# Optimization experiments

Measured on AMD Instinct MI355X. Metric: run time of the kernel, lower is better.

## Reference

```python
import jax, jax.numpy as jnp
import numpy as np

H, KV, HD = 16, 8, 128           # heads, kv heads, head_dim
THETA, EPS = 1.0e6, 1e-6         # rope theta, rmsnorm eps
QMAX = 127.0                     # symmetric int8


def qdq(x):
    """Symmetric int8 fake quant-dequant along last dim (per-token / per-out-channel)."""
    s = jnp.maximum(jnp.max(jnp.abs(x), axis=-1, keepdims=True) / QMAX, 1e-8)
    q = jnp.clip(jnp.round(x / s), -QMAX, QMAX) * s
    return x + jax.lax.stop_gradient(q - x)  # STE


def rms_norm(x, w):
    v = jnp.mean(jnp.square(x.astype(jnp.float32)), axis=-1, keepdims=True)
    return (x.astype(jnp.float32) * jax.lax.rsqrt(v + EPS)).astype(x.dtype) * w


def rotate_half(x):
    x1, x2 = jnp.split(x, 2, axis=-1)
    return jnp.concatenate([-x2, x1], axis=-1)


def setup_inputs() -> dict:
    key = jax.random.key(0)
    ks = jax.random.split(key, 6)
    B, S, D = 1, 2048, 2048
    return {
        "hidden_states": jax.random.normal(ks[0], (B, S, D), jnp.float32),
        "Wq": jax.random.normal(ks[1], (H * HD, D), jnp.float32) * 0.02,
        "Wk": jax.random.normal(ks[2], (KV * HD, D), jnp.float32) * 0.02,
        "Wv": jax.random.normal(ks[3], (KV * HD, D), jnp.float32) * 0.02,
        "Wo": jax.random.normal(ks[4], (D, H * HD), jnp.float32) * 0.02,
        "q_norm_w": jnp.ones((HD,), jnp.float32),
        "k_norm_w": jnp.ones((HD,), jnp.float32),
        "position_ids": jnp.arange(S, dtype=jnp.int32)[None, :],
    }


def reference(hidden_states, Wq, Wk, Wv, Wo, q_norm_w, k_norm_w, position_ids):
    B, S, D = hidden_states.shape
    xq = qdq(hidden_states)                                  # per-token act quant (shared input)
    q = (xq @ qdq(Wq).T).reshape(B, S, H, HD).transpose(0, 2, 1, 3)   # [B,H,S,hd]
    k = (xq @ qdq(Wk).T).reshape(B, S, KV, HD).transpose(0, 2, 1, 3)  # [B,KV,S,hd]
    v = (xq @ qdq(Wv).T).reshape(B, S, KV, HD).transpose(0, 2, 1, 3)

    q = rms_norm(q, q_norm_w)
    k = rms_norm(k, k_norm_w)

    # rotary embeddings
    inv = 1.0 / (THETA ** (jnp.arange(0, HD, 2, dtype=jnp.float32) / HD))
    freqs = position_ids.astype(jnp.float32)[..., None] * inv          # [B,S,hd/2]
    emb = jnp.concatenate([freqs, freqs], axis=-1)                     # [B,S,hd]
    cos = jnp.cos(emb)[:, None].astype(q.dtype)                        # [B,1,S,hd]
    sin = jnp.sin(emb)[:, None].astype(q.dtype)
    q = q * cos + rotate_half(q) * sin
    k = k * cos + rotate_half(k) * sin

    # qkt_matmul.quant_x1 / quant_x2
    q = qdq(q)
    k = qdq(k)

    # GQA repeat
    g = H // KV
    k = jnp.repeat(k, g, axis=1)
    v = jnp.repeat(v, g, axis=1)

    scores = jnp.einsum("bhqd,bhkd->bhqk", q, k) * (HD ** -0.5)       # [B,H,S,S]
    causal = jnp.tril(jnp.ones((S, S), bool))
    scores = jnp.where(causal[None, None], scores, jnp.float32(-1e9))
    p = jax.nn.softmax(scores.astype(jnp.float32), axis=-1).astype(q.dtype)

    # pv_matmul.quant_x1 / quant_x2
    p = qdq(p)
    v = qdq(v)
    attn = jnp.einsum("bhqk,bhkd->bhqd", p, v)                        # [B,H,S,hd]
    attn = attn.transpose(0, 2, 1, 3).reshape(B, S, H * HD)
    return qdq(attn) @ qdq(Wo).T
```

## Files before the change

### kernel.cpp

```cpp
#include <hip/hip_runtime.h>
#include <math.h>

#define NH 16
#define NKV 8
#define HDIM 128
#define SEQ 2048
#define DMODEL 2048

typedef int   v4i __attribute__((ext_vector_type(4)));
typedef float v4f __attribute__((ext_vector_type(4)));
typedef _Float16 v8h __attribute__((ext_vector_type(8)));

static constexpr float SM_SCALE = 0.08838834764831843f;

#define GLOBP(p) (__attribute__((address_space(1))) void*)(p)
#define LDSP(p)  (__attribute__((address_space(3))) void*)(p)
#define ASYNC16(g, l) __builtin_amdgcn_global_load_lds(GLOBP(g), LDSP(l), 16, 0, 0)


__device__ __forceinline__ unsigned short f2h_bits(float x) {
    _Float16 h = (_Float16)x;
    return __builtin_bit_cast(unsigned short, h);
}

__global__ __launch_bounds__(256) void quant_all_k(const float* __restrict__ hidden,
        const float* __restrict__ Wq, const float* __restrict__ Wk,
        const float* __restrict__ Wv, const float* __restrict__ Wo,
        signed char* __restrict__ out, float* __restrict__ scale) {
    int p = blockIdx.x;
    int row0g = p * 16;
    const float* in; int lr0;
    if (row0g < 2048)      { in = hidden; lr0 = row0g; }
    else if (row0g < 4096) { in = Wq; lr0 = row0g - 2048; }
    else if (row0g < 5120) { in = Wk; lr0 = row0g - 4096; }
    else if (row0g < 6144) { in = Wv; lr0 = row0g - 5120; }
    else                   { in = Wo; lr0 = row0g - 6144; }
    const int cols = 2048;
    int tid = threadIdx.x;
    __shared__ float srow[16];
    int r = tid >> 4, l16 = tid & 15;
    const float4* x4 = (const float4*)(in + (size_t)(lr0 + r) * cols);
    float amax = 0.f;
    for (int c4 = l16; c4 < (cols >> 2); c4 += 16) {
        float4 v = x4[c4];
        amax = fmaxf(amax, fmaxf(fmaxf(fabsf(v.x), fabsf(v.y)),
                                 fmaxf(fabsf(v.z), fabsf(v.w))));
    }
#pragma unroll
    for (int m = 1; m <= 8; m <<= 1) amax = fmaxf(amax, __shfl_xor(amax, m));
    if (l16 == 0) {
        float s = fmaxf(amax / 127.0f, 1e-8f);
        srow[r] = s;
        scale[row0g + r] = s;
    }
    __syncthreads();
    int total = (cols >> 4) * 16;
    size_t obase = (size_t)p * 32768;
    for (int idx = tid; idx < total; idx += 256) {
        int f = idx >> 6, q = (idx >> 4) & 3, rr = idx & 15;
        const float* src = in + (size_t)(lr0 + rr) * cols + f * 64 + q * 16;
        float s = srow[rr];
        unsigned int wds[4];
#pragma unroll
        for (int g = 0; g < 4; ++g) {
            float4 v = *(const float4*)(src + g * 4);
            int b0 = (int)fminf(fmaxf(rintf(v.x / s), -127.f), 127.f);
            int b1 = (int)fminf(fmaxf(rintf(v.y / s), -127.f), 127.f);
            int b2 = (int)fminf(fmaxf(rintf(v.z / s), -127.f), 127.f);
            int b3 = (int)fminf(fmaxf(rintf(v.w / s), -127.f), 127.f);
            wds[g] = (b0 & 255) | ((b1 & 255) << 8) | ((b2 & 255) << 16) | ((b3 & 255) << 24);
        }
        *(uint4*)(out + obase + (size_t)idx * 16) =
            make_uint4(wds[0], wds[1], wds[2], wds[3]);
    }
}

__global__ __launch_bounds__(256) void row_quant_k(const float* __restrict__ in,
        signed char* __restrict__ out, float* __restrict__ scale, int cols) {
    int row0 = blockIdx.x * 16;
    int tid = threadIdx.x;
    __shared__ float srow[16];
    int r = tid >> 4, l16 = tid & 15;
    const float4* x4 = (const float4*)(in + (size_t)(row0 + r) * cols);
    float amax = 0.f;
    for (int c4 = l16; c4 < (cols >> 2); c4 += 16) {
        float4 v = x4[c4];
        amax = fmaxf(amax, fmaxf(fmaxf(fabsf(v.x), fabsf(v.y)),
                                 fmaxf(fabsf(v.z), fabsf(v.w))));
    }
#pragma unroll
    for (int m = 1; m <= 8; m <<= 1) amax = fmaxf(amax, __shfl_xor(amax, m));
    if (l16 == 0) {
        float s = fmaxf(amax / 127.0f, 1e-8f);
        srow[r] = s;
        scale[row0 + r] = s;
    }
    __syncthreads();
    int total = (cols >> 4) * 16;
    size_t obase = ((size_t)(row0 >> 4) * (cols >> 6)) << 10;
    for (int idx = tid; idx < total; idx += 256) {
        int f = idx >> 6, q = (idx >> 4) & 3, rr = idx & 15;
        const float* src = in + (size_t)(row0 + rr) * cols + f * 64 + q * 16;
        float s = srow[rr];
        unsigned int wds[4];
#pragma unroll
        for (int g = 0; g < 4; ++g) {
            float4 v = *(const float4*)(src + g * 4);
            int b0 = (int)fminf(fmaxf(rintf(v.x / s), -127.f), 127.f);
            int b1 = (int)fminf(fmaxf(rintf(v.y / s), -127.f), 127.f);
            int b2 = (int)fminf(fmaxf(rintf(v.z / s), -127.f), 127.f);
            int b3 = (int)fminf(fmaxf(rintf(v.w / s), -127.f), 127.f);
            wds[g] = (b0 & 255) | ((b1 & 255) << 8) | ((b2 & 255) << 16) | ((b3 & 255) << 24);
        }
        *(uint4*)(out + obase + (size_t)idx * 16) =
            make_uint4(wds[0], wds[1], wds[2], wds[3]);
    }
}

__global__ __launch_bounds__(256, 3) void gemm_i8_k(const signed char* __restrict__ A,
        const float* __restrict__ sa, const signed char* __restrict__ B,
        const float* __restrict__ sb, float* __restrict__ C, int M, int N, int K) {
    __shared__ __align__(16) signed char lsA[3][8192];
    __shared__ __align__(16) signed char lsB[3][8192];
    int tid = threadIdx.x;
    int w = tid >> 6, l = tid & 63;
    int wr = w >> 1, wc = w & 1;
    int lrow = l & 15;
    int m0 = blockIdx.y * 128, n0 = blockIdx.x * 128;
    int kb6 = K >> 6;
    v4i acc[4][4];
#pragma unroll
    for (int i = 0; i < 4; ++i)
#pragma unroll
        for (int j = 0; j < 4; ++j) acc[i][j] = (v4i){0, 0, 0, 0};

    auto stage = [&](int buf, int k6) {
#pragma unroll
        for (int a = 0; a < 2; ++a) {
            int f = a * 4 + w;
            ASYNC16(A + (((size_t)(((m0 >> 4) + f) * kb6 + k6)) << 10) + l * 16,
                    lsA[buf] + f * 1024);
            ASYNC16(B + (((size_t)(((n0 >> 4) + f) * kb6 + k6)) << 10) + l * 16,
                    lsB[buf] + f * 1024);
        }
    };

    stage(0, 0);
    if (kb6 > 1) {
        stage(1, 1);
        asm volatile("s_waitcnt vmcnt(4)" ::: "memory");
    } else {
        asm volatile("s_waitcnt vmcnt(0)" ::: "memory");
    }
    __builtin_amdgcn_s_barrier();
    for (int t = 0; t < kb6; ++t) {
        if (t + 2 < kb6) stage((t + 2) % 3, t + 2);
        int cur = t % 3;
        v4i af[4], bf[4];
#pragma unroll
        for (int i = 0; i < 4; ++i) af[i] = *(const v4i*)(lsA[cur] + (wr * 4 + i) * 1024 + l * 16);
#pragma unroll
        for (int j = 0; j < 4; ++j) bf[j] = *(const v4i*)(lsB[cur] + (wc * 4 + j) * 1024 + l * 16);
#pragma unroll
        for (int i = 0; i < 4; ++i)
#pragma unroll
            for (int j = 0; j < 4; ++j)
                acc[i][j] = __builtin_amdgcn_mfma_i32_16x16x64_i8(af[i], bf[j], acc[i][j], 0, 0, 0);
        if (t + 2 < kb6) asm volatile("s_waitcnt vmcnt(4)" ::: "memory");
        else             asm volatile("s_waitcnt vmcnt(0)" ::: "memory");
        __builtin_amdgcn_s_barrier();
    }
    int r0 = m0 + wr * 64, c0 = n0 + wc * 64;
    int lg = l >> 4;
    float sbv[4];
#pragma unroll
    for (int j = 0; j < 4; ++j) sbv[j] = sb[c0 + j * 16 + lrow];
#pragma unroll
    for (int i = 0; i < 4; ++i) {
        float4 s4 = *(const float4*)(sa + r0 + i * 16 + lg * 4);
        float sav[4] = {s4.x, s4.y, s4.z, s4.w};
#pragma unroll
        for (int j = 0; j < 4; ++j) {
#pragma unroll
            for (int reg = 0; reg < 4; ++reg) {
                int rr = r0 + i * 16 + lg * 4 + reg;
                C[(size_t)rr * N + c0 + j * 16 + lrow] = (float)acc[i][j][reg] * (sav[reg] * sbv[j]);
            }
        }
    }
}

__global__ void rope_init_k(float* __restrict__ inv_tab) {
    int i = threadIdx.x;
    inv_tab[i] = 1.0f / (float)pow(1.0e6, (double)i / 64.0);
}
__global__ void rope_tab_k(const int* __restrict__ pos_ids, const float* __restrict__ inv_tab,
                           float* __restrict__ ct, float* __restrict__ st) {
    int t = blockIdx.x;
    int fi = threadIdx.x;
    float fr = (float)pos_ids[t] * inv_tab[fi];
    float sn, c;
    sincosf(fr, &sn, &c);
    ct[t * 64 + fi] = c;
    st[t * 64 + fi] = sn;
}

__global__ __launch_bounds__(256) void qkv_post_k(const float* __restrict__ qkv_lin,
        const float* __restrict__ qw, const float* __restrict__ kw,
        const float* __restrict__ ct, const float* __restrict__ st,
        signed char* __restrict__ q_i8, float* __restrict__ sq,
        signed char* __restrict__ k_i8, float* __restrict__ sk) {
    int t = blockIdx.x;
    int wv = threadIdx.x >> 6, l = threadIdx.x & 63;
    const float* row = qkv_lin + (size_t)t * 4096;
    float cth = ct[t * 64 + l];
    float sth = st[t * 64 + l];
    size_t ta0 = (size_t)(((t >> 4) * 2) << 10)
               + (size_t)((((l >> 4) & 3) << 8) + ((t & 15) << 4) + (l & 15));
    for (int slot = wv; slot < 24; slot += 4) {
        float x0 = row[slot * 128 + l];
        float x1 = row[slot * 128 + l + 64];
        float ss = x0 * x0 + x1 * x1;
#pragma unroll
        for (int m = 1; m <= 32; m <<= 1) ss += __shfl_xor(ss, m);
        float rs = 1.0f / sqrtf(ss / 128.0f + 1e-6f);
        const float* wn = (slot < 16) ? qw : kw;
        x0 = (x0 * rs) * wn[l];
        x1 = (x1 * rs) * wn[l + 64];
        float nx0 = x0 * cth - x1 * sth;
        float nx1 = x1 * cth + x0 * sth;
        x0 = nx0; x1 = nx1;
        float amax = fmaxf(fabsf(x0), fabsf(x1));
#pragma unroll
        for (int m = 1; m <= 32; m <<= 1) amax = fmaxf(amax, __shfl_xor(amax, m));
        float s = fmaxf(amax / 127.0f, 1e-8f);
        float q0 = fminf(fmaxf(rintf(x0 / s), -127.f), 127.f);
        float q1 = fminf(fmaxf(rintf(x1 / s), -127.f), 127.f);
        if (slot < 16) {
            signed char* dst = q_i8 + (size_t)slot * (SEQ * 128);
            dst[ta0] = (signed char)(int)q0;
            dst[ta0 + 1024] = (signed char)(int)q1;
            if (l == 0) sq[slot * SEQ + t] = s;
        } else {
            signed char* dst = k_i8 + (size_t)(slot - 16) * (SEQ * 128);
            dst[ta0] = (signed char)(int)q0;
            dst[ta0 + 1024] = (signed char)(int)q1;
            if (l == 0) sk[(slot - 16) * SEQ + t] = s;
        }
    }
}

__global__ __launch_bounds__(256) void vt_split_k(const float* __restrict__ qkv_lin,
        unsigned short* __restrict__ vtT) {
    int kv = blockIdx.y, kb = blockIdx.x;
    int t0 = kb * 64;
    __shared__ float tile[64][132];
    __shared__ float srow[64];
    int tid = threadIdx.x;
    const float* src = qkv_lin + (size_t)t0 * 4096 + 3072 + kv * 128;
#pragma unroll
    for (int i = 0; i < 8; ++i) {
        int f4 = i * 256 + tid;
        int r = f4 >> 5, c = (f4 & 31) << 2;
        float4 v = *(const float4*)(src + (size_t)r * 4096 + c);
        tile[r][c] = v.x; tile[r][c + 1] = v.y; tile[r][c + 2] = v.z; tile[r][c + 3] = v.w;
    }
    __syncthreads();
    {
        int r = tid >> 2, qq = tid & 3;
        float amax = 0.f;
#pragma unroll
        for (int e = 0; e < 32; ++e) amax = fmaxf(amax, fabsf(tile[r][qq * 32 + e]));
        amax = fmaxf(amax, __shfl_xor(amax, 1));
        amax = fmaxf(amax, __shfl_xor(amax, 2));
        if (qq == 0) srow[r] = fmaxf(amax / 127.0f, 1e-8f);
    }
    __syncthreads();
    int d = tid >> 1, th = (tid & 1) * 32;
    size_t base = (size_t)kv * (SEQ * 128);
#pragma unroll
    for (int j = 0; j < 32; j += 2) {
        int tl = th + j;
        float s0 = srow[tl], s1 = srow[tl + 1];
        float a = fminf(fmaxf(rintf(tile[tl][d] / s0), -127.f), 127.f) * s0;
        float b = fminf(fmaxf(rintf(tile[tl + 1][d] / s1), -127.f), 127.f) * s1;
        unsigned int ua = f2h_bits(a), ub = f2h_bits(b);
        int off = kb * 8192 + ((d >> 4) * 2 + ((tl >> 5) & 1)) * 512
                + (((d & 15) + (((tl >> 3) & 3) << 4)) << 3) + (tl & 7);
        *(unsigned int*)(vtT + base + off) = ua | (ub << 16);
    }
}

__global__ __launch_bounds__(256, 4) void attn_p1_k(const signed char* __restrict__ q_i8,
        const float* __restrict__ sq, const signed char* __restrict__ k_i8,
        const float* __restrict__ sk, float* __restrict__ mm) {
    int bx = blockIdx.x, hp = blockIdx.y;
    int qb = 31 - (bx >> 2), c = bx & 3;
    int nch = (qb + 8) >> 3;
    if (c >= nch) return;
    int q0 = qb * 64;
    int kb0 = c * 8, kb1 = min((c + 1) * 8, qb + 1);
    int tid = threadIdx.x, w = tid >> 6, l = tid & 63;
    int lrow = l & 15, lg = l >> 4;
    int h0 = hp * 2, h1 = h0 + 1;

    const signed char* qtA = q_i8 + (size_t)h0 * (SEQ * 128)
                           + ((size_t)((((q0 >> 4) + w) * 2)) << 10) + l * 16;
    const signed char* qtB = qtA + (size_t)(SEQ * 128);
    v4i qfA0 = *(const v4i*)(qtA), qfA1 = *(const v4i*)(qtA + 1024);
    v4i qfB0 = *(const v4i*)(qtB), qfB1 = *(const v4i*)(qtB + 1024);
    float4 sA = *(const float4*)(sq + (size_t)h0 * SEQ + q0 + w * 16 + lg * 4);
    float4 sB = *(const float4*)(sq + (size_t)h1 * SEQ + q0 + w * 16 + lg * 4);
    float sqrA[4] = {sA.x, sA.y, sA.z, sA.w};
    float sqrB[4] = {sB.x, sB.y, sB.z, sB.w};
    const signed char* kbase = k_i8 + (size_t)hp * (SEQ * 128);
    const float* skb = sk + (size_t)hp * SEQ;

    float mA[4], mB[4];
#pragma unroll
    for (int r = 0; r < 4; ++r) { mA[r] = -1e30f; mB[r] = -1e30f; }

    v4i ka[8], kn[8];
    float skc[4], skn[4];
    auto loadK = [&](v4i* dst, float* sdst, int k0) {
#pragma unroll
        for (int f = 0; f < 8; ++f)
            dst[f] = *(const v4i*)(kbase + ((size_t)((k0 >> 4) * 2 + f) << 10) + l * 16);
#pragma unroll
        for (int j = 0; j < 4; ++j) sdst[j] = skb[k0 + j * 16 + lrow];
    };

    loadK(ka, skc, kb0 * 64);
    for (int kb = kb0; kb < kb1; ++kb) {
        if (kb + 1 < kb1) loadK(kn, skn, (kb + 1) * 64);
        int k0 = kb * 64;
        v4i sciA[4], sciB[4];
#pragma unroll
        for (int j = 0; j < 4; ++j) {
            v4i z = {0, 0, 0, 0};
            v4i tA = __builtin_amdgcn_mfma_i32_16x16x64_i8(qfA0, ka[j * 2], z, 0, 0, 0);
            sciA[j] = __builtin_amdgcn_mfma_i32_16x16x64_i8(qfA1, ka[j * 2 + 1], tA, 0, 0, 0);
            v4i tB = __builtin_amdgcn_mfma_i32_16x16x64_i8(qfB0, ka[j * 2], z, 0, 0, 0);
            sciB[j] = __builtin_amdgcn_mfma_i32_16x16x64_i8(qfB1, ka[j * 2 + 1], tB, 0, 0, 0);
        }
#pragma unroll
        for (int reg = 0; reg < 4; ++reg) {
            int r = q0 + w * 16 + lg * 4 + reg;
#pragma unroll
            for (int j = 0; j < 4; ++j) {
                bool ok = (k0 + j * 16 + lrow <= r);
                float ss = skc[j] * SM_SCALE;
                float svA = ((float)sciA[j][reg] * sqrA[reg]) * ss;
                float svB = ((float)sciB[j][reg] * sqrB[reg]) * ss;
                mA[reg] = fmaxf(mA[reg], ok ? svA : -1e30f);
                mB[reg] = fmaxf(mB[reg], ok ? svB : -1e30f);
            }
        }
        if (kb + 1 < kb1) {
#pragma unroll
            for (int f = 0; f < 8; ++f) ka[f] = kn[f];
#pragma unroll
            for (int j = 0; j < 4; ++j) skc[j] = skn[j];
        }
    }
#pragma unroll
    for (int reg = 0; reg < 4; ++reg) {
#pragma unroll
        for (int mask = 1; mask <= 8; mask <<= 1) {
            mA[reg] = fmaxf(mA[reg], __shfl_xor(mA[reg], mask));
            mB[reg] = fmaxf(mB[reg], __shfl_xor(mB[reg], mask));
        }
    }
    if (lrow == 0) {
        size_t bA = ((size_t)(h0 * 32 + qb) * 4 + c) * 64;
        size_t bB = ((size_t)(h1 * 32 + qb) * 4 + c) * 64;
#pragma unroll
        for (int reg = 0; reg < 4; ++reg) {
            mm[bA + w * 16 + lg * 4 + reg] = mA[reg];
            mm[bB + w * 16 + lg * 4 + reg] = mB[reg];
        }
    }
}

__global__ __launch_bounds__(256, 2) void attn_p2_k(const signed char* __restrict__ q_i8,
        const float* __restrict__ sq, const signed char* __restrict__ k_i8,
        const float* __restrict__ sk, const unsigned short* __restrict__ vtT,
        const float* __restrict__ mm, float* __restrict__ attn2, float* __restrict__ pp,
        float* __restrict__ zb) {
    __shared__ __align__(16) unsigned short vlds[3][8192];
    __shared__ __align__(16) signed char klds[2][8192];
    __shared__ __align__(16) unsigned short plds[4096];
    __shared__ __align__(16) float slds[1024];
    int bx = blockIdx.x, hp = blockIdx.y;
    int qb = 31 - (bx >> 1), c = bx & 1;
    int nch2 = (qb >= 16) ? 2 : 1;
    if (c >= nch2) return;
    int q0 = qb * 64;
    int kb0 = c * 16, kb1 = min((c + 1) * 16, qb + 1);
    int tid = threadIdx.x, w = tid >> 6, l = tid & 63;
    int lrow = l & 15, lg = l >> 4;
    int h0 = hp * 2, h1 = h0 + 1;

    const signed char* qtA = q_i8 + (size_t)h0 * (SEQ * 128)
                           + ((size_t)((((q0 >> 4) + w) * 2)) << 10) + l * 16;
    const signed char* qtB = qtA + (size_t)(SEQ * 128);
    v4i qfA0 = *(const v4i*)(qtA), qfA1 = *(const v4i*)(qtA + 1024);
    v4i qfB0 = *(const v4i*)(qtB), qfB1 = *(const v4i*)(qtB + 1024);
    float4 sA = *(const float4*)(sq + (size_t)h0 * SEQ + q0 + w * 16 + lg * 4);
    float4 sB = *(const float4*)(sq + (size_t)h1 * SEQ + q0 + w * 16 + lg * 4);
    float sqrA[4] = {sA.x, sA.y, sA.z, sA.w};
    float sqrB[4] = {sB.x, sB.y, sB.z, sB.w};

    int nch1 = (qb + 8) >> 3;
    float mfA[4], mfB[4];
#pragma unroll
    for (int reg = 0; reg < 4; ++reg) {
        int r = w * 16 + lg * 4 + reg;
        float MA = -1e30f, MB = -1e30f;
        for (int c1 = 0; c1 < nch1; ++c1) {
            MA = fmaxf(MA, mm[((size_t)(h0 * 32 + qb) * 4 + c1) * 64 + r]);
            MB = fmaxf(MB, mm[((size_t)(h1 * 32 + qb) * 4 + c1) * 64 + r]);
        }
        mfA[reg] = MA; mfB[reg] = MB;
    }

    const signed char* kbase = k_i8 + (size_t)hp * (SEQ * 128);
    const float* skb = sk + (size_t)hp * SEQ;
    const unsigned short* vt = vtT + (size_t)hp * (SEQ * 128);

    auto issueV = [&](int kb) {
        unsigned short* vb = &vlds[kb % 3][0];
#pragma unroll
        for (int a = 0; a < 4; ++a) {
            int fv = a * 4 + w;
            ASYNC16(vt + (size_t)kb * 8192 + fv * 512 + l * 8, vb + fv * 512);
        }
    };
    auto issueK = [&](int kb) {
        signed char* kbuf = &klds[kb & 1][0];
#pragma unroll
        for (int a = 0; a < 2; ++a) {
            int f = a * 4 + w;
            ASYNC16(kbase + ((size_t)(kb * 8 + f) << 10) + l * 16, kbuf + f * 1024);
        }
    };

    v4f accA[8], accB[8];
#pragma unroll
    for (int jd = 0; jd < 8; ++jd) {
        accA[jd] = (v4f){0.f, 0.f, 0.f, 0.f};
        accB[jd] = (v4f){0.f, 0.f, 0.f, 0.f};
    }
    float ztA[4] = {0.f, 0.f, 0.f, 0.f};
    float ztB[4] = {0.f, 0.f, 0.f, 0.f};

    ASYNC16(skb + kb0 * 64 + w * 256 + l * 4, (char*)slds + w * 1024);
    issueK(kb0);
    issueV(kb0);
    if (kb0 + 1 < kb1) {
        issueV(kb0 + 1);
        asm volatile("s_waitcnt vmcnt(4)" ::: "memory");
    } else {
        asm volatile("s_waitcnt vmcnt(0)" ::: "memory");
    }
    __builtin_amdgcn_s_barrier();

    for (int kb = kb0; kb < kb1; ++kb) {
        int k0 = kb * 64;
        if (kb + 1 < kb1) issueK(kb + 1);
        if (kb + 2 < kb1) issueV(kb + 2);
        v4i ka[8];
#pragma unroll
        for (int f = 0; f < 8; ++f)
            ka[f] = *(const v4i*)(&klds[kb & 1][0] + f * 1024 + l * 16);
        float skc[4];
#pragma unroll
        for (int j = 0; j < 4; ++j) skc[j] = slds[(kb - kb0) * 64 + j * 16 + lrow];
        v4i sciA[4], sciB[4];
#pragma unroll
        for (int j = 0; j < 4; ++j) {
            v4i z = {0, 0, 0, 0};
            v4i tA = __builtin_amdgcn_mfma_i32_16x16x64_i8(qfA0, ka[j * 2], z, 0, 0, 0);
            sciA[j] = __builtin_amdgcn_mfma_i32_16x16x64_i8(qfA1, ka[j * 2 + 1], tA, 0, 0, 0);
            v4i tB = __builtin_amdgcn_mfma_i32_16x16x64_i8(qfB0, ka[j * 2], z, 0, 0, 0);
            sciB[j] = __builtin_amdgcn_mfma_i32_16x16x64_i8(qfB1, ka[j * 2 + 1], tB, 0, 0, 0);
        }
#pragma unroll
        for (int reg = 0; reg < 4; ++reg) {
            int rq = lg * 4 + reg;
            int r = q0 + w * 16 + rq;
#pragma unroll
            for (int j = 0; j < 4; ++j) {
                int cc = j * 16 + lrow;
                float pd = 0.f;
                if (k0 + cc <= r) {
                    float sv = ((float)sciA[j][reg] * (sqrA[reg] * skc[j])) * SM_SCALE;
                    float e = __expf(sv - mfA[reg]);
                    ztA[reg] += e;
                    pd = fminf(rintf(127.0f * e), 127.f);
                }
                plds[(w * 2 + (cc >> 5)) * 512 + (rq + 16 * ((cc >> 3) & 3)) * 8 + (cc & 7)] =
                    f2h_bits(pd);
            }
        }
        v8h pfA0 = *(const v8h*)(plds + (w * 2 + 0) * 512 + l * 8);
        v8h pfA1 = *(const v8h*)(plds + (w * 2 + 1) * 512 + l * 8);
#pragma unroll
        for (int reg = 0; reg < 4; ++reg) {
            int rq = lg * 4 + reg;
            int r = q0 + w * 16 + rq;
#pragma unroll
            for (int j = 0; j < 4; ++j) {
                int cc = j * 16 + lrow;
                float pd = 0.f;
                if (k0 + cc <= r) {
                    float sv = ((float)sciB[j][reg] * (sqrB[reg] * skc[j])) * SM_SCALE;
                    float e = __expf(sv - mfB[reg]);
                    ztB[reg] += e;
                    pd = fminf(rintf(127.0f * e), 127.f);
                }
                plds[(w * 2 + (cc >> 5)) * 512 + (rq + 16 * ((cc >> 3) & 3)) * 8 + (cc & 7)] =
                    f2h_bits(pd);
            }
        }
        v8h pfB0 = *(const v8h*)(plds + (w * 2 + 0) * 512 + l * 8);
        v8h pfB1 = *(const v8h*)(plds + (w * 2 + 1) * 512 + l * 8);
        const unsigned short* vb = &vlds[kb % 3][0];
#pragma unroll
        for (int jd = 0; jd < 8; ++jd) {
            v8h vh0 = *(const v8h*)(vb + (jd * 2 + 0) * 512 + l * 8);
            v8h vh1 = *(const v8h*)(vb + (jd * 2 + 1) * 512 + l * 8);
            v4f tA = accA[jd];
            tA = __builtin_amdgcn_mfma_f32_16x16x32_f16(pfA0, vh0, tA, 0, 0, 0);
            tA = __builtin_amdgcn_mfma_f32_16x16x32_f16(pfA1, vh1, tA, 0, 0, 0);
            accA[jd] = tA;
            v4f tB = accB[jd];
            tB = __builtin_amdgcn_mfma_f32_16x16x32_f16(pfB0, vh0, tB, 0, 0, 0);
            tB = __builtin_amdgcn_mfma_f32_16x16x32_f16(pfB1, vh1, tB, 0, 0, 0);
            accB[jd] = tB;
        }
        if (kb + 2 < kb1) asm volatile("s_waitcnt vmcnt(4)" ::: "memory");
        else              asm volatile("s_waitcnt vmcnt(0)" ::: "memory");
        __builtin_amdgcn_s_barrier();
    }
#pragma unroll
    for (int reg = 0; reg < 4; ++reg) {
#pragma unroll
        for (int mask = 1; mask <= 8; mask <<= 1) {
            ztA[reg] += __shfl_xor(ztA[reg], mask);
            ztB[reg] += __shfl_xor(ztB[reg], mask);
        }
    }
    if (qb < 16) {
        float spA[4], spB[4];
#pragma unroll
        for (int reg = 0; reg < 4; ++reg) {
            spA[reg] = fmaxf((1.0f / ztA[reg]) / 127.0f, 1e-8f);
            spB[reg] = fmaxf((1.0f / ztB[reg]) / 127.0f, 1e-8f);
        }
#pragma unroll
        for (int jd = 0; jd < 8; ++jd)
#pragma unroll
            for (int reg = 0; reg < 4; ++reg) {
                int r = q0 + w * 16 + lg * 4 + reg;
                attn2[(size_t)r * DMODEL + h0 * HDIM + jd * 16 + lrow] = accA[jd][reg] * spA[reg];
                attn2[(size_t)r * DMODEL + h1 * HDIM + jd * 16 + lrow] = accB[jd][reg] * spB[reg];
            }
    } else {
        if (c == 0) {
#pragma unroll
            for (int jd = 0; jd < 8; ++jd)
#pragma unroll
                for (int reg = 0; reg < 4; ++reg) {
                    int r = q0 + w * 16 + lg * 4 + reg;
                    attn2[(size_t)r * DMODEL + h0 * HDIM + jd * 16 + lrow] = accA[jd][reg];
                    attn2[(size_t)r * DMODEL + h1 * HDIM + jd * 16 + lrow] = accB[jd][reg];
                }
        } else {
#pragma unroll
            for (int jd = 0; jd < 8; ++jd)
#pragma unroll
                for (int reg = 0; reg < 4; ++reg) {
                    int rr = w * 16 + lg * 4 + reg;
                    pp[(((size_t)h0 * 16 + (qb - 16)) * 64 + rr) * 128 + jd * 16 + lrow] = accA[jd][reg];
                    pp[(((size_t)h1 * 16 + (qb - 16)) * 64 + rr) * 128 + jd * 16 + lrow] = accB[jd][reg];
                }
        }
        if (lrow == 0) {
            size_t zA = (((size_t)h0 * 16 + (qb - 16)) * 2 + c) * 64;
            size_t zB = (((size_t)h1 * 16 + (qb - 16)) * 2 + c) * 64;
#pragma unroll
            for (int reg = 0; reg < 4; ++reg) {
                zb[zA + w * 16 + lg * 4 + reg] = ztA[reg];
                zb[zB + w * 16 + lg * 4 + reg] = ztB[reg];
            }
        }
    }
}

__global__ __launch_bounds__(256) void attn_red_k(float* __restrict__ attn2,
        const float* __restrict__ pp, const float* __restrict__ zb) {
    int t16 = blockIdx.x, h = blockIdx.y;
    int qb = t16 + 16;
    int tid = threadIdx.x;
    for (int e = tid; e < 2048; e += 256) {
        int i = (e * 4) >> 7, j = (e * 4) & 127;
        float z0 = zb[(((size_t)h * 16 + t16) * 2 + 0) * 64 + i];
        float z1 = zb[(((size_t)h * 16 + t16) * 2 + 1) * 64 + i];
        float zinv = 1.0f / (z0 + z1);
        float spv = fmaxf(zinv / 127.0f, 1e-8f);
        float4 p = *(const float4*)&pp[(((size_t)h * 16 + t16) * 64 + i) * 128 + j];
        float* d = &attn2[(size_t)(qb * 64 + i) * DMODEL + h * HDIM + j];
        float4 dv = *(float4*)d;
        dv.x = (dv.x + p.x) * spv; dv.y = (dv.y + p.y) * spv;
        dv.z = (dv.z + p.z) * spv; dv.w = (dv.w + p.w) * spv;
        *(float4*)d = dv;
    }
}

extern "C" void kernel_launch(void* const* d_in, const int* in_sizes, int n_in,
                              void* d_out, int out_size, void* d_ws, size_t ws_size,
                              hipStream_t stream) {
    (void)in_sizes; (void)n_in; (void)out_size; (void)ws_size;
    const float* hidden = (const float*)d_in[0];
    const float* Wq = (const float*)d_in[1];
    const float* Wk = (const float*)d_in[2];
    const float* Wv = (const float*)d_in[3];
    const float* Wo = (const float*)d_in[4];
    const float* qw = (const float*)d_in[5];
    const float* kw = (const float*)d_in[6];
    const int* pos = (const int*)d_in[7];
    float* out = (float*)d_out;
    char* ws = (char*)d_ws;

    const size_t MB = 1024 * 1024;
    signed char* x_i8  = (signed char*)(ws);
    signed char* wq_i8 = (signed char*)(ws + 4 * MB);
    signed char* wo_i8 = (signed char*)(ws + 12 * MB);
    signed char* q_i8  = (signed char*)(ws + 16 * MB);
    signed char* k_i8  = (signed char*)(ws + 20 * MB);
    float* sx  = (float*)(ws + 22 * MB);
    float* swq = sx + 2048;
    float* swo = sx + 6144;
    float* sq  = sx + 8192;
    float* sk  = sq + NH * SEQ;
    float* sa  = sk + NKV * SEQ;
    float* inv_tab = sa + 2048;
    float* ct  = (float*)(ws + 22 * MB + 512 * 1024);
    float* st  = (float*)(ws + 22 * MB + 1024 * 1024);
    float* qkv_lin = (float*)(ws + 24 * MB);
    float* attn2 = (float*)(ws + 32 * MB);
    float* pp    = (float*)(ws + 48 * MB);
    unsigned short* vtT = (unsigned short*)(ws + 56 * MB);
    float* mm    = (float*)(ws + 60 * MB);
    float* zb    = (float*)(ws + 60 * MB + 512 * 1024);
    signed char* a_i8 = x_i8;

    rope_init_k<<<1, 64, 0, stream>>>(inv_tab);
    rope_tab_k<<<2048, 64, 0, stream>>>(pos, inv_tab, ct, st);
    quant_all_k<<<512, 256, 0, stream>>>(hidden, Wq, Wk, Wv, Wo, x_i8, sx);

    gemm_i8_k<<<dim3(32, 16), 256, 0, stream>>>(x_i8, sx, wq_i8, swq, qkv_lin, 2048, 4096, 2048);

    qkv_post_k<<<2048, 256, 0, stream>>>(qkv_lin, qw, kw, ct, st, q_i8, sq, k_i8, sk);
    vt_split_k<<<dim3(32, 8), 256, 0, stream>>>(qkv_lin, vtT);

    attn_p1_k<<<dim3(128, 8), 256, 0, stream>>>(q_i8, sq, k_i8, sk, mm);
    attn_p2_k<<<dim3(64, 8), 256, 0, stream>>>(q_i8, sq, k_i8, sk, vtT, mm, attn2, pp, zb);
    attn_red_k<<<dim3(16, 16), 256, 0, stream>>>(attn2, pp, zb);

    row_quant_k<<<128, 256, 0, stream>>>(attn2, a_i8, sa, 2048);
    gemm_i8_k<<<dim3(16, 16), 256, 0, stream>>>(a_i8, sa, wo_i8, swo, out, 2048, 2048, 2048);
}
```

Baseline: 197.4 us.

## Fuse QKV GEMM epilogue with norm, RoPE, quantization and V transpose

Replaces the generic int8 QKV GEMM plus separate qkv_post and vt_split kernels with one GEMM kernel. Its epilogue stages each 128x128 fp32 tile in shared memory and applies RMSNorm, RoPE and int8 quantization for Q/K, or fake-quant and the fp16 transposed layout for V. It also folds the inverse-frequency table into the rope table kernel. This removes the 32 MB fp32 qkv_lin round trip and two launches, at the cost of about 67 KB of shared memory per block and a serialized epilogue that may lower occupancy.

```diff
diff --git a/kernel.cpp b/kernel.cpp
--- a/kernel.cpp
+++ b/kernel.cpp
@@ -190,105 +190,158 @@
     }
 }
 
-__global__ void rope_init_k(float* __restrict__ inv_tab) {
-    int i = threadIdx.x;
-    inv_tab[i] = 1.0f / (float)pow(1.0e6, (double)i / 64.0);
-}
-__global__ void rope_tab_k(const int* __restrict__ pos_ids, const float* __restrict__ inv_tab,
+__global__ __launch_bounds__(256, 2) void gemm_qkv_k(const signed char* __restrict__ A,
+        const float* __restrict__ sa, const signed char* __restrict__ B,
+        const float* __restrict__ sb,
+        const float* __restrict__ qw, const float* __restrict__ kw,
+        const float* __restrict__ ct, const float* __restrict__ st,
+        signed char* __restrict__ q_i8, float* __restrict__ sq,
+        signed char* __restrict__ k_i8, float* __restrict__ sk,
+        unsigned short* __restrict__ vtT) {
+    __shared__ __align__(16) char smem[68608];
+    signed char (*lsA)[8192] = (signed char(*)[8192])smem;
+    signed char (*lsB)[8192] = (signed char(*)[8192])(smem + 24576);
+    float (*tile)[132] = (float(*)[132])smem;
+    float* srow = (float*)(smem + 67584);
+    int tid = threadIdx.x;
+    int w = tid >> 6, l = tid & 63;
+    int wr = w >> 1, wc = w & 1;
+    int lrow = l & 15, lg = l >> 4;
+    int m0 = blockIdx.y * 128, n0 = blockIdx.x * 128;
+    const int kb6 = 32;
+    v4i acc[4][4];
+#pragma unroll
+    for (int i = 0; i < 4; ++i)
+#pragma unroll
+        for (int j = 0; j < 4; ++j) acc[i][j] = (v4i){0, 0, 0, 0};
+
+    auto stage = [&](int buf, int k6) {
+#pragma unroll
+        for (int a = 0; a < 2; ++a) {
+            int f = a * 4 + w;
+            ASYNC16(A + (((size_t)(((m0 >> 4) + f) * kb6 + k6)) << 10) + l * 16,
+                    lsA[buf] + f * 1024);
+            ASYNC16(B + (((size_t)(((n0 >> 4) + f) * kb6 + k6)) << 10) + l * 16,
+                    lsB[buf] + f * 1024);
+        }
+    };
+
+    stage(0, 0);
+    stage(1, 1);
+    asm volatile("s_waitcnt vmcnt(4)" ::: "memory");
+    __builtin_amdgcn_s_barrier();
+    for (int t = 0; t < kb6; ++t) {
+        if (t + 2 < kb6) stage((t + 2) % 3, t + 2);
+        int cur = t % 3;
+        v4i af[4], bf[4];
+#pragma unroll
+        for (int i = 0; i < 4; ++i) af[i] = *(const v4i*)(lsA[cur] + (wr * 4 + i) * 1024 + l * 16);
+#pragma unroll
+        for (int j = 0; j < 4; ++j) bf[j] = *(const v4i*)(lsB[cur] + (wc * 4 + j) * 1024 + l * 16);
+#pragma unroll
+        for (int i = 0; i < 4; ++i)
+#pragma unroll
+            for (int j = 0; j < 4; ++j)
+                acc[i][j] = __builtin_amdgcn_mfma_i32_16x16x64_i8(af[i], bf[j], acc[i][j], 0, 0, 0);
+        if (t + 2 < kb6) asm volatile("s_waitcnt vmcnt(4)" ::: "memory");
+        else             asm volatile("s_waitcnt vmcnt(0)" ::: "memory");
+        __builtin_amdgcn_s_barrier();
+    }
+    {
+        int c0 = n0 + wc * 64;
+        float sbv[4];
+#pragma unroll
+        for (int j = 0; j < 4; ++j) sbv[j] = sb[c0 + j * 16 + lrow];
+#pragma unroll
+        for (int i = 0; i < 4; ++i) {
+            float4 s4 = *(const float4*)(sa + m0 + wr * 64 + i * 16 + lg * 4);
+            float sav[4] = {s4.x, s4.y, s4.z, s4.w};
+#pragma unroll
+            for (int j = 0; j < 4; ++j)
+#pragma unroll
+                for (int reg = 0; reg < 4; ++reg)
+                    tile[wr * 64 + i * 16 + lg * 4 + reg][wc * 64 + j * 16 + lrow] =
+                        (float)acc[i][j][reg] * (sav[reg] * sbv[j]);
+        }
+    }
+    __syncthreads();
+    int slot = n0 >> 7;
+    if (slot < 24) {
+        const float* wn = (slot < 16) ? qw : kw;
+        signed char* dst8 = (slot < 16) ? q_i8 + (size_t)slot * (SEQ * 128)
+                                        : k_i8 + (size_t)(slot - 16) * (SEQ * 128);
+        float* sdst = (slot < 16) ? sq + (size_t)slot * SEQ : sk + (size_t)(slot - 16) * SEQ;
+        float wn0 = wn[l], wn1 = wn[l + 64];
+        for (int it = 0; it < 32; ++it) {
+            int tl = it * 4 + w;
+            int t = m0 + tl;
+            float x0 = tile[tl][l];
+            float x1 = tile[tl][l + 64];
+            float ss = x0 * x0 + x1 * x1;
+#pragma unroll
+            for (int m = 1; m <= 32; m <<= 1) ss += __shfl_xor(ss, m);
+            float rs = 1.0f / sqrtf(ss / 128.0f + 1e-6f);
+            x0 = (x0 * rs) * wn0;
+            x1 = (x1 * rs) * wn1;
+            float cth = ct[t * 64 + l];
+            float sth = st[t * 64 + l];
+            float nx0 = x0 * cth - x1 * sth;
+            float nx1 = x1 * cth + x0 * sth;
+            float amax = fmaxf(fabsf(nx0), fabsf(nx1));
+#pragma unroll
+            for (int m = 1; m <= 32; m <<= 1) amax = fmaxf(amax, __shfl_xor(amax, m));
+            float s = fmaxf(amax / 127.0f, 1e-8f);
+            float q0 = fminf(fmaxf(rintf(nx0 / s), -127.f), 127.f);
+            float q1 = fminf(fmaxf(rintf(nx1 / s), -127.f), 127.f);
+            size_t ta0 = (size_t)(((t >> 4) * 2) << 10)
+                       + (size_t)((((l >> 4) & 3) << 8) + ((t & 15) << 4) + (l & 15));
+            dst8[ta0] = (signed char)(int)q0;
+            dst8[ta0 + 1024] = (signed char)(int)q1;
+            if (l == 0) sdst[t] = s;
+        }
+    } else {
+        int kv = slot - 24;
+        for (int it = 0; it < 32; ++it) {
+            int tl = it * 4 + w;
+            float x0 = tile[tl][l];
+            float x1 = tile[tl][l + 64];
+            float amax = fmaxf(fabsf(x0), fabsf(x1));
+#pragma unroll
+            for (int m = 1; m <= 32; m <<= 1) amax = fmaxf(amax, __shfl_xor(amax, m));
+            if (l == 0) srow[tl] = fmaxf(amax / 127.0f, 1e-8f);
+        }
+        __syncthreads();
+        int d = tid >> 1, th = (tid & 1) * 32;
+        size_t base = (size_t)kv * (SEQ * 128);
+#pragma unroll
+        for (int kbl = 0; kbl < 2; ++kbl) {
+            int kb = (m0 >> 6) + kbl;
+#pragma unroll
+            for (int j = 0; j < 32; j += 2) {
+                int t64 = th + j;
+                int tg = kbl * 64 + t64;
+                float s0 = srow[tg], s1 = srow[tg + 1];
+                float a = fminf(fmaxf(rintf(tile[tg][d] / s0), -127.f), 127.f) * s0;
+                float b = fminf(fmaxf(rintf(tile[tg + 1][d] / s1), -127.f), 127.f) * s1;
+                unsigned int ua = f2h_bits(a), ub = f2h_bits(b);
+                int off = kb * 8192 + ((d >> 4) * 2 + ((t64 >> 5) & 1)) * 512
+                        + (((d & 15) + (((t64 >> 3) & 3) << 4)) << 3) + (t64 & 7);
+                *(unsigned int*)(vtT + base + off) = ua | (ub << 16);
+            }
+        }
+    }
+}
+
+__global__ void rope_tab_k(const int* __restrict__ pos_ids,
                            float* __restrict__ ct, float* __restrict__ st) {
     int t = blockIdx.x;
     int fi = threadIdx.x;
-    float fr = (float)pos_ids[t] * inv_tab[fi];
+    float inv = 1.0f / (float)pow(1.0e6, (double)fi / 64.0);
+    float fr = (float)pos_ids[t] * inv;
     float sn, c;
     sincosf(fr, &sn, &c);
     ct[t * 64 + fi] = c;
     st[t * 64 + fi] = sn;
-}
-
-__global__ __launch_bounds__(256) void qkv_post_k(const float* __restrict__ qkv_lin,
-        const float* __restrict__ qw, const float* __restrict__ kw,
-        const float* __restrict__ ct, const float* __restrict__ st,
-        signed char* __restrict__ q_i8, float* __restrict__ sq,
-        signed char* __restrict__ k_i8, float* __restrict__ sk) {
-    int t = blockIdx.x;
-    int wv = threadIdx.x >> 6, l = threadIdx.x & 63;
-    const float* row = qkv_lin + (size_t)t * 4096;
-    float cth = ct[t * 64 + l];
-    float sth = st[t * 64 + l];
-    size_t ta0 = (size_t)(((t >> 4) * 2) << 10)
-               + (size_t)((((l >> 4) & 3) << 8) + ((t & 15) << 4) + (l & 15));
-    for (int slot = wv; slot < 24; slot += 4) {
-        float x0 = row[slot * 128 + l];
-        float x1 = row[slot * 128 + l + 64];
-        float ss = x0 * x0 + x1 * x1;
-#pragma unroll
-        for (int m = 1; m <= 32; m <<= 1) ss += __shfl_xor(ss, m);
-        float rs = 1.0f / sqrtf(ss / 128.0f + 1e-6f);
-        const float* wn = (slot < 16) ? qw : kw;
-        x0 = (x0 * rs) * wn[l];
-        x1 = (x1 * rs) * wn[l + 64];
-        float nx0 = x0 * cth - x1 * sth;
-        float nx1 = x1 * cth + x0 * sth;
-        x0 = nx0; x1 = nx1;
-        float amax = fmaxf(fabsf(x0), fabsf(x1));
-#pragma unroll
-        for (int m = 1; m <= 32; m <<= 1) amax = fmaxf(amax, __shfl_xor(amax, m));
-        float s = fmaxf(amax / 127.0f, 1e-8f);
-        float q0 = fminf(fmaxf(rintf(x0 / s), -127.f), 127.f);
-        float q1 = fminf(fmaxf(rintf(x1 / s), -127.f), 127.f);
-        if (slot < 16) {
-            signed char* dst = q_i8 + (size_t)slot * (SEQ * 128);
-            dst[ta0] = (signed char)(int)q0;
-            dst[ta0 + 1024] = (signed char)(int)q1;
-            if (l == 0) sq[slot * SEQ + t] = s;
-        } else {
-            signed char* dst = k_i8 + (size_t)(slot - 16) * (SEQ * 128);
-            dst[ta0] = (signed char)(int)q0;
-            dst[ta0 + 1024] = (signed char)(int)q1;
-            if (l == 0) sk[(slot - 16) * SEQ + t] = s;
-        }
-    }
-}
-
-__global__ __launch_bounds__(256) void vt_split_k(const float* __restrict__ qkv_lin,
-        unsigned short* __restrict__ vtT) {
-    int kv = blockIdx.y, kb = blockIdx.x;
-    int t0 = kb * 64;
-    __shared__ float tile[64][132];
-    __shared__ float srow[64];
-    int tid = threadIdx.x;
-    const float* src = qkv_lin + (size_t)t0 * 4096 + 3072 + kv * 128;
-#pragma unroll
-    for (int i = 0; i < 8; ++i) {
-        int f4 = i * 256 + tid;
-        int r = f4 >> 5, c = (f4 & 31) << 2;
-        float4 v = *(const float4*)(src + (size_t)r * 4096 + c);
-        tile[r][c] = v.x; tile[r][c + 1] = v.y; tile[r][c + 2] = v.z; tile[r][c + 3] = v.w;
-    }
-    __syncthreads();
-    {
-        int r = tid >> 2, qq = tid & 3;
-        float amax = 0.f;
-#pragma unroll
-        for (int e = 0; e < 32; ++e) amax = fmaxf(amax, fabsf(tile[r][qq * 32 + e]));
-        amax = fmaxf(amax, __shfl_xor(amax, 1));
-        amax = fmaxf(amax, __shfl_xor(amax, 2));
-        if (qq == 0) srow[r] = fmaxf(amax / 127.0f, 1e-8f);
-    }
-    __syncthreads();
-    int d = tid >> 1, th = (tid & 1) * 32;
-    size_t base = (size_t)kv * (SEQ * 128);
-#pragma unroll
-    for (int j = 0; j < 32; j += 2) {
-        int tl = th + j;
-        float s0 = srow[tl], s1 = srow[tl + 1];
-        float a = fminf(fmaxf(rintf(tile[tl][d] / s0), -127.f), 127.f) * s0;
-        float b = fminf(fmaxf(rintf(tile[tl + 1][d] / s1), -127.f), 127.f) * s1;
-        unsigned int ua = f2h_bits(a), ub = f2h_bits(b);
-        int off = kb * 8192 + ((d >> 4) * 2 + ((tl >> 5) & 1)) * 512
-                + (((d & 15) + (((tl >> 3) & 3) << 4)) << 3) + (tl & 7);
-        *(unsigned int*)(vtT + base + off) = ua | (ub << 16);
-    }
 }
 
 __global__ __launch_bounds__(256, 4) void attn_p1_k(const signed char* __restrict__ q_i8,
@@ -645,10 +698,8 @@
     float* sq  = sx + 8192;
     float* sk  = sq + NH * SEQ;
     float* sa  = sk + NKV * SEQ;
-    float* inv_tab = sa + 2048;
     float* ct  = (float*)(ws + 22 * MB + 512 * 1024);
     float* st  = (float*)(ws + 22 * MB + 1024 * 1024);
-    float* qkv_lin = (float*)(ws + 24 * MB);
     float* attn2 = (float*)(ws + 32 * MB);
     float* pp    = (float*)(ws + 48 * MB);
     unsigned short* vtT = (unsigned short*)(ws + 56 * MB);
@@ -656,14 +707,11 @@
     float* zb    = (float*)(ws + 60 * MB + 512 * 1024);
     signed char* a_i8 = x_i8;
 
-    rope_init_k<<<1, 64, 0, stream>>>(inv_tab);
-    rope_tab_k<<<2048, 64, 0, stream>>>(pos, inv_tab, ct, st);
+    rope_tab_k<<<2048, 64, 0, stream>>>(pos, ct, st);
     quant_all_k<<<512, 256, 0, stream>>>(hidden, Wq, Wk, Wv, Wo, x_i8, sx);
 
-    gemm_i8_k<<<dim3(32, 16), 256, 0, stream>>>(x_i8, sx, wq_i8, swq, qkv_lin, 2048, 4096, 2048);
-
-    qkv_post_k<<<2048, 256, 0, stream>>>(qkv_lin, qw, kw, ct, st, q_i8, sq, k_i8, sk);
-    vt_split_k<<<dim3(32, 8), 256, 0, stream>>>(qkv_lin, vtT);
+    gemm_qkv_k<<<dim3(32, 16), 256, 0, stream>>>(x_i8, sx, wq_i8, swq, qw, kw, ct, st,
+                                                 q_i8, sq, k_i8, sk, vtT);
 
     attn_p1_k<<<dim3(128, 8), 256, 0, stream>>>(q_i8, sq, k_i8, sk, mm);
     attn_p2_k<<<dim3(64, 8), 256, 0, stream>>>(q_i8, sq, k_i8, sk, vtT, mm, attn2, pp, zb);
```

After: 194.2 us. About the same (-1.7%).
